# Kernel tuning notes

Measured on AMD Instinct MI355X. Metric: run time of the kernel, lower is better.

Reference implementation:

```python
import jax, jax.numpy as jnp
import numpy as np
import math

D_IN = 1024
D_OUT = 1024
NUM_HEADS = 16
HEAD_DIM = D_OUT // NUM_HEADS
B = 2
S = 4096


def setup_inputs() -> dict:
    key = jax.random.key(0)
    ks = jax.random.split(key, 6)
    x = jax.random.normal(ks[0], (B, S, D_IN), dtype=jnp.float32)
    # kaiming-uniform-ish scale for weights; exact init values don't matter for correctness
    bound = 1.0 / math.sqrt(D_IN)
    Wq = jax.random.uniform(ks[1], (D_OUT, D_IN), minval=-bound, maxval=bound, dtype=jnp.float32)
    Wk = jax.random.uniform(ks[2], (D_OUT, D_IN), minval=-bound, maxval=bound, dtype=jnp.float32)
    Wv = jax.random.uniform(ks[3], (D_OUT, D_IN), minval=-bound, maxval=bound, dtype=jnp.float32)
    Wo = jax.random.uniform(ks[4], (D_OUT, D_OUT), minval=-bound, maxval=bound, dtype=jnp.float32)
    bo = jax.random.uniform(ks[5], (D_OUT,), minval=-bound, maxval=bound, dtype=jnp.float32)
    return {"x": x, "Wq": Wq, "Wk": Wk, "Wv": Wv, "Wo": Wo, "bo": bo}


@jax.custom_vjp
def binarize(w):
    return jnp.sign(w)

def _bin_fwd(w):
    return jnp.sign(w), w

def _bin_bwd(w, g):
    # straight-through estimator: pass grad where |w| <= 1
    return (g * (jnp.abs(w) <= 1).astype(g.dtype),)

binarize.defvjp(_bin_fwd, _bin_bwd)


def reference(x, Wq, Wk, Wv, Wo, bo):
    b, n, _ = x.shape
    h, hd = NUM_HEADS, HEAD_DIM
    # binarized projections (torch F.linear: x @ W.T)
    q = (x @ binarize(Wq).T).reshape(b, n, h, hd).transpose(0, 2, 1, 3)  # [b,h,n,hd]
    k = (x @ binarize(Wk).T).reshape(b, n, h, hd).transpose(0, 2, 1, 3)
    v = (x @ binarize(Wv).T).reshape(b, n, h, hd).transpose(0, 2, 1, 3)
    scores = jnp.einsum('bhqd,bhkd->bhqk', q, k) / math.sqrt(hd)  # [b,h,n,n]
    causal = jnp.tril(jnp.ones((n, n), dtype=bool))
    scores = jnp.where(causal, scores, -jnp.inf)
    attn = jax.nn.softmax(scores, axis=-1)
    # dropout p=0.0 -> identity
    ctx = jnp.einsum('bhqk,bhkd->bqhd', attn, v).reshape(b, n, h * hd)
    return ctx @ binarize(Wo).T + bo
```

## Files before the change

kernel.cpp:

```cpp
#include <hip/hip_runtime.h>
#include <hip/hip_bf16.h>
#include <cstdint>
#include <cstddef>

#define S 4096
#define D 1024
#define H 16
#define HD 64
#define BATCH 2
#define M_TOK 8192
#define K2 2048

typedef short short8 __attribute__((ext_vector_type(8)));
typedef __bf16 bf16x8 __attribute__((ext_vector_type(8)));
typedef float f32x4 __attribute__((ext_vector_type(4)));
typedef unsigned int u32;

static __device__ __forceinline__ ushort f2bf(float f) {
  union { float f; uint32_t u; } v; v.f = f;
  uint32_t u = v.u + 0x7FFFu + ((v.u >> 16) & 1u);
  return (ushort)(u >> 16);
}
static __device__ __forceinline__ float bf2f(ushort h) {
  union { uint32_t u; float f; } v; v.u = ((uint32_t)h) << 16; return v.f;
}
static __device__ __forceinline__ uint32_t cvtpk(float lo, float hi) {
  uint32_t r;
  asm("v_cvt_pk_bf16_f32 %0, %1, %2" : "=v"(r) : "v"(lo), "v"(hi));
  return r;
}
static __device__ __forceinline__ float vexp2(float x) {
  float r;
  asm("v_exp_f32 %0, %1" : "=v"(r) : "v"(x));
  return r;
}
static __device__ __forceinline__ bf16x8 pack4(uint32_t a, uint32_t b, uint32_t c, uint32_t d) {
  union { uint32_t u[4]; bf16x8 v; } z;
  z.u[0] = a; z.u[1] = b; z.u[2] = c; z.u[3] = d;
  return z.v;
}
static __device__ __forceinline__ void gld16(const void* g, void* l) {
  __builtin_amdgcn_global_load_lds(
      (const __attribute__((address_space(1))) u32*)g,
      (__attribute__((address_space(3))) u32*)l, 16, 0, 0);
}
static __device__ __forceinline__ ushort sgn(float a) {
  return a > 0.f ? 0x3F80 : (a < 0.f ? 0xBF80 : 0);
}

__global__ void prep_x(const float* __restrict__ x, ushort* __restrict__ xcat) {
  int i = blockIdx.x * blockDim.x + threadIdx.x;
  const int total = M_TOK * 128;
  for (; i < total; i += gridDim.x * blockDim.x) {
    int row = i >> 7, c8 = (i & 127) * 8;
    const float* px = &x[(size_t)row * 1024 + c8];
    float4 a = *(const float4*)px;
    float4 b = *(const float4*)(px + 4);
    float va[8] = {a.x, a.y, a.z, a.w, b.x, b.y, b.z, b.w};
    union { ushort u[8]; short8 v; } Hh, Ll;
#pragma unroll
    for (int j = 0; j < 8; ++j) {
      ushort h = f2bf(va[j]);
      Hh.u[j] = h;
      Ll.u[j] = f2bf(va[j] - bf2f(h));
    }
    *(short8*)&xcat[(size_t)row * K2 + c8] = Hh.v;
    *(short8*)&xcat[(size_t)row * K2 + 1024 + c8] = Ll.v;
  }
}

__global__ void prep_w(const float* __restrict__ wq, const float* __restrict__ wk,
                       const float* __restrict__ wv, const float* __restrict__ wo,
                       ushort* __restrict__ wcat, ushort* __restrict__ wob) {
  int i = blockIdx.x * blockDim.x + threadIdx.x;
  const int total = (D * D) / 4;
  for (; i < total; i += gridDim.x * blockDim.x) {
    float4 a;
    union { ushort u[4]; uint2 v; } t;
    a = *(const float4*)&wq[i * 4];
    t.u[0] = sgn(a.x); t.u[1] = sgn(a.y); t.u[2] = sgn(a.z); t.u[3] = sgn(a.w);
    *(uint2*)&wcat[i * 4] = t.v;
    a = *(const float4*)&wk[i * 4];
    t.u[0] = sgn(a.x); t.u[1] = sgn(a.y); t.u[2] = sgn(a.z); t.u[3] = sgn(a.w);
    *(uint2*)&wcat[D * D + i * 4] = t.v;
    a = *(const float4*)&wv[i * 4];
    t.u[0] = sgn(a.x); t.u[1] = sgn(a.y); t.u[2] = sgn(a.z); t.u[3] = sgn(a.w);
    *(uint2*)&wcat[2 * D * D + i * 4] = t.v;
    a = *(const float4*)&wo[i * 4];
    t.u[0] = sgn(a.x); t.u[1] = sgn(a.y); t.u[2] = sgn(a.z); t.u[3] = sgn(a.w);
    *(uint2*)&wob[i * 4] = t.v;
  }
}

template<int EPI, int KK, int BROW>
__global__ __launch_bounds__(256) void gemm97(
    const ushort* __restrict__ A, const ushort* __restrict__ Bw,
    ushort* __restrict__ q_hi, ushort* __restrict__ q_lo,
    ushort* __restrict__ k_hi, ushort* __restrict__ k_lo,
    ushort* __restrict__ v_t,
    float* __restrict__ of, const float* __restrict__ bias)
{
  __shared__ ushort smA[128 * 32];
  __shared__ ushort smB[128 * 32];
  const int tid = threadIdx.x;
  const int l = tid & 63;
  const int w = tid >> 6;
  const int x = l & 15, g = l >> 4;
  const int wm = w >> 1, wn = w & 1;
  const int bm = blockIdx.x, bn = blockIdx.y;

  const ushort* gA[2]; const ushort* gB[2]; int ldso[2];
#pragma unroll
  for (int p = 0; p < 2; ++p) {
    int q = p * 256 + tid;
    gA[p] = &A[(size_t)(bm * 128 + (q >> 2)) * KK + (q & 3) * 8];
    gB[p] = &Bw[(size_t)(bn * 128 + (q >> 2)) * BROW + (q & 3) * 8];
    ldso[p] = (p * 256 + w * 64) * 8;
  }

  f32x4 acc[4][4] = {};

  for (int k0 = 0; k0 < KK; k0 += 32) {
    __syncthreads();
#pragma unroll
    for (int p = 0; p < 2; ++p) {
      gld16(gA[p] + k0, &smA[ldso[p]]);
      gld16(gB[p] + (k0 & (BROW - 1)), &smB[ldso[p]]);
    }
    __syncthreads();
    bf16x8 af[4], bf_[4];
#pragma unroll
    for (int m = 0; m < 4; ++m)
      af[m] = *(const bf16x8*)&smA[(wm * 64 + m * 16 + x) * 32 + g * 8];
#pragma unroll
    for (int n = 0; n < 4; ++n)
      bf_[n] = *(const bf16x8*)&smB[(wn * 64 + n * 16 + x) * 32 + g * 8];
#pragma unroll
    for (int m = 0; m < 4; ++m)
#pragma unroll
      for (int n = 0; n < 4; ++n)
        acc[m][n] = __builtin_amdgcn_mfma_f32_16x16x32_bf16(af[m], bf_[n], acc[m][n], 0, 0, 0);
  }

  if (EPI == 0) {
    const int proj = bn >> 3;
    ushort* oh = (proj == 0) ? q_hi : k_hi;
    ushort* ol = (proj == 0) ? q_lo : k_lo;
#pragma unroll
    for (int m = 0; m < 4; ++m)
#pragma unroll
      for (int n = 0; n < 4; ++n)
#pragma unroll
        for (int r = 0; r < 4; ++r) {
          int rowg = bm * 128 + wm * 64 + m * 16 + g * 4 + r;
          int colg = bn * 128 + wn * 64 + n * 16 + x;
          float v = acc[m][n][r];
          int bi = rowg >> 12, ntok = rowg & 4095;
          int cg = colg & 1023;
          int h = cg >> 6, hd = cg & 63;
          size_t bhb = (size_t)(bi * H + h) * (S * HD);
          if (proj < 2) {
            size_t off = bhb + (size_t)ntok * HD + hd;
            ushort hiv = f2bf(v);
            oh[off] = hiv;
            ol[off] = f2bf(v - bf2f(hiv));
          } else {
            int t5 = ntok & 31;
            int pos = ((t5 >> 2) & 3) * 8 + ((t5 >> 4) & 1) * 4 + (t5 & 3);
            v_t[bhb + (size_t)hd * S + (ntok & ~31) + pos] = f2bf(v);
          }
        }
  } else {
#pragma unroll
    for (int m = 0; m < 4; ++m)
#pragma unroll
      for (int n = 0; n < 4; ++n)
#pragma unroll
        for (int r = 0; r < 4; ++r) {
          int rowg = bm * 128 + wm * 64 + m * 16 + g * 4 + r;
          int colg = bn * 128 + wn * 64 + n * 16 + x;
          of[(size_t)rowg * D + colg] = acc[m][n][r] + bias[colg];
        }
  }
}

__global__ __launch_bounds__(256) void flash5(
    const ushort* __restrict__ qhi, const ushort* __restrict__ qlo,
    const ushort* __restrict__ khi, const ushort* __restrict__ klo,
    const ushort* __restrict__ vt, ushort* __restrict__ ctx)
{
  __shared__ ushort smKhi[2][64 * 64];
  __shared__ ushort smKlo[2][64 * 64];
  __shared__ ushort smVT[2][64 * 64];

  const int tid = threadIdx.x;
  const int l = tid & 63;
  const int w = tid >> 6;
  const int x = l & 15;
  const int g = l >> 4;
  const int bh = blockIdx.x;
  const int qt = (int)(gridDim.y - 1) - (int)blockIdx.y;
  const int qbase = qt * 128;
  const size_t qkbase = (size_t)bh * S * HD;

  int soff_k[2]; size_t soff_v[2]; int ldso[2];
#pragma unroll
  for (int p = 0; p < 2; ++p) {
    int q = p * 256 + tid;
    int rr = q >> 3;
    int sb = (q & 7) ^ (rr & 7);
    soff_k[p] = rr * HD + sb * 8;
    soff_v[p] = (size_t)rr * S + sb * 8;
    ldso[p] = (p * 256 + w * 64) * 8;
  }
  const ushort* khb = khi + qkbase;
  const ushort* klb = klo + qkbase;
  const ushort* vtb = vt + qkbase;

  bf16x8 bq[2][2][2];
#pragma unroll
  for (int qs = 0; qs < 2; ++qs) {
    int qrow = qbase + w * 32 + qs * 16 + x;
    size_t base = qkbase + (size_t)qrow * HD + g * 8;
    bq[qs][0][0] = *(const bf16x8*)&qhi[base];
    bq[qs][0][1] = *(const bf16x8*)&qhi[base + 32];
    bq[qs][1][0] = *(const bf16x8*)&qlo[base];
    bq[qs][1][1] = *(const bf16x8*)&qlo[base + 32];
  }

  float mrun[2] = {-1e30f, -1e30f};
  float lrun[2] = {0.f, 0.f};
  f32x4 oacc[2][4] = {};

  const int kvmax = (qbase + 127) >> 6;
  const int qmaxw = qbase + w * 32 + 31;
  const float C1 = 0.125f * 1.44269504f;
  const float TH = 8.0f / C1;

#pragma unroll
  for (int p = 0; p < 2; ++p) {
    gld16(khb + soff_k[p], &smKhi[0][ldso[p]]);
    gld16(klb + soff_k[p], &smKlo[0][ldso[p]]);
    gld16(vtb + soff_v[p], &smVT[0][ldso[p]]);
  }
  __syncthreads();

  int cur = 0;
  for (int kv = 0; kv <= kvmax; ++kv) {
    if (kv < kvmax) {
      const ushort* kh = khb + (size_t)(kv + 1) * (64 * HD);
      const ushort* kl = klb + (size_t)(kv + 1) * (64 * HD);
      const ushort* vp = vtb + (size_t)(kv + 1) * 64;
      int nb = cur ^ 1;
#pragma unroll
      for (int p = 0; p < 2; ++p) {
        gld16(kh + soff_k[p], &smKhi[nb][ldso[p]]);
        gld16(kl + soff_k[p], &smKlo[nb][ldso[p]]);
        gld16(vp + soff_v[p], &smVT[nb][ldso[p]]);
      }
    }

    if (kv * 64 <= qmaxw) {
      const ushort* bKhi = smKhi[cur];
      const ushort* bKlo = smKlo[cur];
      const ushort* bVT = smVT[cur];

      f32x4 scq[2][4];
      __builtin_amdgcn_s_setprio(1);
#pragma unroll
      for (int t = 0; t < 4; ++t) {
        f32x4 a0 = {}, a1 = {};
#pragma unroll
        for (int c = 0; c < 2; ++c) {
          int pb = (t * 16 + x) * 64 + ((4 * c + g) ^ (x & 7)) * 8;
          bf16x8 kH = *(const bf16x8*)&bKhi[pb];
          bf16x8 kL = *(const bf16x8*)&bKlo[pb];
          a0 = __builtin_amdgcn_mfma_f32_16x16x32_bf16(kH, bq[0][0][c], a0, 0, 0, 0);
          a0 = __builtin_amdgcn_mfma_f32_16x16x32_bf16(kL, bq[0][0][c], a0, 0, 0, 0);
          a0 = __builtin_amdgcn_mfma_f32_16x16x32_bf16(kH, bq[0][1][c], a0, 0, 0, 0);
          a1 = __builtin_amdgcn_mfma_f32_16x16x32_bf16(kH, bq[1][0][c], a1, 0, 0, 0);
          a1 = __builtin_amdgcn_mfma_f32_16x16x32_bf16(kL, bq[1][0][c], a1, 0, 0, 0);
          a1 = __builtin_amdgcn_mfma_f32_16x16x32_bf16(kH, bq[1][1][c], a1, 0, 0, 0);
        }
        scq[0][t] = a0; scq[1][t] = a1;
      }
      __builtin_amdgcn_s_setprio(0);

      const bool needmask = (kv * 64 + 63 > qbase + w * 32);
      uint32_t pbq[2][2][4];

#pragma unroll
      for (int qs = 0; qs < 2; ++qs) {
        if (needmask) {
          int qglob = qbase + w * 32 + qs * 16 + x;
          int kb = kv * 64 + 4 * g;
#pragma unroll
          for (int t = 0; t < 4; ++t)
#pragma unroll
            for (int r = 0; r < 4; ++r)
              if (kb + t * 16 + r > qglob) scq[qs][t][r] = -1e30f;
        }
        float mt[4];
#pragma unroll
        for (int t = 0; t < 4; ++t)
          mt[t] = fmaxf(fmaxf(scq[qs][t][0], scq[qs][t][1]),
                        fmaxf(scq[qs][t][2], scq[qs][t][3]));
        float mloc = fmaxf(fmaxf(mt[0], mt[1]), fmaxf(mt[2], mt[3]));
        if (__any(mloc > mrun[qs] + TH)) {
          mloc = fmaxf(mloc, __shfl_xor(mloc, 16));
          mloc = fmaxf(mloc, __shfl_xor(mloc, 32));
          float mnew = fmaxf(mrun[qs], mloc);
          float scal = vexp2((mrun[qs] - mnew) * C1);
          mrun[qs] = mnew;
          lrun[qs] *= scal;
#pragma unroll
          for (int dt = 0; dt < 4; ++dt) oacc[qs][dt] *= scal;
        }
        float mc = mrun[qs] * C1;
#pragma unroll
        for (int t = 0; t < 4; ++t)
#pragma unroll
          for (int r = 0; r < 4; ++r)
            scq[qs][t][r] = vexp2(scq[qs][t][r] * C1 - mc);
        float st[4];
#pragma unroll
        for (int t = 0; t < 4; ++t)
          st[t] = (scq[qs][t][0] + scq[qs][t][1]) + (scq[qs][t][2] + scq[qs][t][3]);
        lrun[qs] += (st[0] + st[1]) + (st[2] + st[3]);
#pragma unroll
        for (int c = 0; c < 2; ++c) {
          pbq[qs][c][0] = cvtpk(scq[qs][2 * c][0], scq[qs][2 * c][1]);
          pbq[qs][c][1] = cvtpk(scq[qs][2 * c][2], scq[qs][2 * c][3]);
          pbq[qs][c][2] = cvtpk(scq[qs][2 * c + 1][0], scq[qs][2 * c + 1][1]);
          pbq[qs][c][3] = cvtpk(scq[qs][2 * c + 1][2], scq[qs][2 * c + 1][3]);
        }
      }

      __builtin_amdgcn_s_setprio(1);
#pragma unroll
      for (int c = 0; c < 2; ++c)
#pragma unroll
        for (int dt = 0; dt < 4; ++dt) {
          bf16x8 vf = *(const bf16x8*)&bVT[(dt * 16 + x) * 64 + ((4 * c + g) ^ (x & 7)) * 8];
          oacc[0][dt] = __builtin_amdgcn_mfma_f32_16x16x32_bf16(
              vf, pack4(pbq[0][c][0], pbq[0][c][1], pbq[0][c][2], pbq[0][c][3]), oacc[0][dt], 0, 0, 0);
          oacc[1][dt] = __builtin_amdgcn_mfma_f32_16x16x32_bf16(
              vf, pack4(pbq[1][c][0], pbq[1][c][1], pbq[1][c][2], pbq[1][c][3]), oacc[1][dt], 0, 0, 0);
        }
      __builtin_amdgcn_s_setprio(0);
    }

    __syncthreads();
    cur ^= 1;
  }

  const int b = bh >> 4, h = bh & 15;
#pragma unroll
  for (int qs = 0; qs < 2; ++qs) {
    float ls = lrun[qs];
    ls += __shfl_xor(ls, 16);
    ls += __shfl_xor(ls, 32);
    float inv = 1.0f / ls;
    int tok = qbase + w * 32 + qs * 16 + x;
#pragma unroll
    for (int dt = 0; dt < 4; ++dt) {
      uint2 uu;
      uu.x = cvtpk(oacc[qs][dt][0] * inv, oacc[qs][dt][1] * inv);
      uu.y = cvtpk(oacc[qs][dt][2] * inv, oacc[qs][dt][3] * inv);
      *(uint2*)&ctx[(size_t)(b * S + tok) * D + h * 64 + dt * 16 + 4 * g] = uu;
    }
  }
}

extern "C" void kernel_launch(void* const* d_in, const int* in_sizes, int n_in,
                              void* d_out, int out_size, void* d_ws, size_t ws_size,
                              hipStream_t stream) {
  const float* x  = (const float*)d_in[0];
  const float* Wq = (const float*)d_in[1];
  const float* Wk = (const float*)d_in[2];
  const float* Wv = (const float*)d_in[3];
  const float* Wo = (const float*)d_in[4];
  const float* bo = (const float*)d_in[5];
  float* out = (float*)d_out;

  if (ws_size < (size_t)120 * 1024 * 1024) return;

  char* ws = (char*)d_ws;
  const size_t MB = 1024 * 1024;
  ushort* xcat = (ushort*)(ws);
  ushort* ctx  = (ushort*)(ws);
  ushort* wcat = (ushort*)(ws + 32 * MB);
  ushort* wob  = (ushort*)(ws + 38 * MB);
  ushort* qhi  = (ushort*)(ws + 40 * MB);
  ushort* qlo  = (ushort*)(ws + 56 * MB);
  ushort* khi  = (ushort*)(ws + 72 * MB);
  ushort* klo  = (ushort*)(ws + 88 * MB);
  ushort* vt   = (ushort*)(ws + 104 * MB);

  prep_x<<<2048, 256, 0, stream>>>(x, xcat);
  prep_w<<<1024, 256, 0, stream>>>(Wq, Wk, Wv, Wo, wcat, wob);

  gemm97<0, K2, 1024><<<dim3(64, 24), 256, 0, stream>>>(
      xcat, wcat, qhi, qlo, khi, klo, vt, nullptr, nullptr);

  flash5<<<dim3(BATCH * H, S / 128), 256, 0, stream>>>(qhi, qlo, khi, klo, vt, ctx);

  gemm97<2, 1024, 1024><<<dim3(64, 8), 256, 0, stream>>>(
      ctx, wob, nullptr, nullptr, nullptr, nullptr, nullptr, out, bo);
}
```

Before: 339.3 us.

## Pair complementary causal query tiles in one 512-thread flash block

Each flash-attention block now has 8 waves. Waves 0-3 handle query tile p and waves 4-7 handle tile 31-p, so every block does balanced causal work and the shared K/V tiles are loaded cooperatively across twice as many threads. This targets the load imbalance and tail effect of the triangular causal workload and halves the grid size. In exchange, waves on the short tile sit idle through the later KV iterations while still joining the barriers, and launch bounds now require 512 threads with 4 blocks per SM.

Measured after the change: 362.3 us. 1.07x slower.

```diff
diff --git a/kernel.cpp b/kernel.cpp
--- a/kernel.cpp
+++ b/kernel.cpp
@@ -184,7 +184,7 @@
   }
 }
 
-__global__ __launch_bounds__(256) void flash5(
+__global__ __launch_bounds__(512, 4) void flash6(
     const ushort* __restrict__ qhi, const ushort* __restrict__ qlo,
     const ushort* __restrict__ khi, const ushort* __restrict__ klo,
     const ushort* __restrict__ vt, ushort* __restrict__ ctx)
@@ -196,23 +196,21 @@
   const int tid = threadIdx.x;
   const int l = tid & 63;
   const int w = tid >> 6;
+  const int wl = w & 3;
   const int x = l & 15;
   const int g = l >> 4;
   const int bh = blockIdx.x;
-  const int qt = (int)(gridDim.y - 1) - (int)blockIdx.y;
-  const int qbase = qt * 128;
+  const int p = blockIdx.y;
+  const int qtw = (w < 4) ? p : (31 - p);
+  const int qbase = qtw * 128;
   const size_t qkbase = (size_t)bh * S * HD;
 
-  int soff_k[2]; size_t soff_v[2]; int ldso[2];
-#pragma unroll
-  for (int p = 0; p < 2; ++p) {
-    int q = p * 256 + tid;
-    int rr = q >> 3;
-    int sb = (q & 7) ^ (rr & 7);
-    soff_k[p] = rr * HD + sb * 8;
-    soff_v[p] = (size_t)rr * S + sb * 8;
-    ldso[p] = (p * 256 + w * 64) * 8;
-  }
+  const int rr = tid >> 3;
+  const int sb = (tid & 7) ^ (rr & 7);
+  const int soff_k = rr * HD + sb * 8;
+  const size_t soff_v = (size_t)rr * S + sb * 8;
+  const int ldso = w * 512;
+
   const ushort* khb = khi + qkbase;
   const ushort* klb = klo + qkbase;
   const ushort* vtb = vt + qkbase;
@@ -220,7 +218,7 @@
   bf16x8 bq[2][2][2];
 #pragma unroll
   for (int qs = 0; qs < 2; ++qs) {
-    int qrow = qbase + w * 32 + qs * 16 + x;
+    int qrow = qbase + wl * 32 + qs * 16 + x;
     size_t base = qkbase + (size_t)qrow * HD + g * 8;
     bq[qs][0][0] = *(const bf16x8*)&qhi[base];
     bq[qs][0][1] = *(const bf16x8*)&qhi[base + 32];
@@ -232,17 +230,14 @@
   float lrun[2] = {0.f, 0.f};
   f32x4 oacc[2][4] = {};
 
-  const int kvmax = (qbase + 127) >> 6;
-  const int qmaxw = qbase + w * 32 + 31;
+  const int kvmax = 2 * (31 - p) + 1;
+  const int qmaxw = qbase + wl * 32 + 31;
   const float C1 = 0.125f * 1.44269504f;
   const float TH = 8.0f / C1;
 
-#pragma unroll
-  for (int p = 0; p < 2; ++p) {
-    gld16(khb + soff_k[p], &smKhi[0][ldso[p]]);
-    gld16(klb + soff_k[p], &smKlo[0][ldso[p]]);
-    gld16(vtb + soff_v[p], &smVT[0][ldso[p]]);
-  }
+  gld16(khb + soff_k, &smKhi[0][ldso]);
+  gld16(klb + soff_k, &smKlo[0][ldso]);
+  gld16(vtb + soff_v, &smVT[0][ldso]);
   __syncthreads();
 
   int cur = 0;
@@ -252,12 +247,9 @@
       const ushort* kl = klb + (size_t)(kv + 1) * (64 * HD);
       const ushort* vp = vtb + (size_t)(kv + 1) * 64;
       int nb = cur ^ 1;
-#pragma unroll
-      for (int p = 0; p < 2; ++p) {
-        gld16(kh + soff_k[p], &smKhi[nb][ldso[p]]);
-        gld16(kl + soff_k[p], &smKlo[nb][ldso[p]]);
-        gld16(vp + soff_v[p], &smVT[nb][ldso[p]]);
-      }
+      gld16(kh + soff_k, &smKhi[nb][ldso]);
+      gld16(kl + soff_k, &smKlo[nb][ldso]);
+      gld16(vp + soff_v, &smVT[nb][ldso]);
     }
 
     if (kv * 64 <= qmaxw) {
@@ -286,13 +278,13 @@
       }
       __builtin_amdgcn_s_setprio(0);
 
-      const bool needmask = (kv * 64 + 63 > qbase + w * 32);
+      const bool needmask = (kv * 64 + 63 > qbase + wl * 32);
       uint32_t pbq[2][2][4];
 
 #pragma unroll
       for (int qs = 0; qs < 2; ++qs) {
         if (needmask) {
-          int qglob = qbase + w * 32 + qs * 16 + x;
+          int qglob = qbase + wl * 32 + qs * 16 + x;
           int kb = kv * 64 + 4 * g;
 #pragma unroll
           for (int t = 0; t < 4; ++t)
@@ -361,7 +353,7 @@
     ls += __shfl_xor(ls, 16);
     ls += __shfl_xor(ls, 32);
     float inv = 1.0f / ls;
-    int tok = qbase + w * 32 + qs * 16 + x;
+    int tok = qbase + wl * 32 + qs * 16 + x;
 #pragma unroll
     for (int dt = 0; dt < 4; ++dt) {
       uint2 uu;
@@ -403,7 +395,7 @@
   gemm97<0, K2, 1024><<<dim3(64, 24), 256, 0, stream>>>(
       xcat, wcat, qhi, qlo, khi, klo, vt, nullptr, nullptr);
 
-  flash5<<<dim3(BATCH * H, S / 128), 256, 0, stream>>>(qhi, qlo, khi, klo, vt, ctx);
+  flash6<<<dim3(BATCH * H, 16), 512, 0, stream>>>(qhi, qlo, khi, klo, vt, ctx);
 
   gemm97<2, 1024, 1024><<<dim3(64, 8), 256, 0, stream>>>(
       ctx, wob, nullptr, nullptr, nullptr, nullptr, nullptr, out, bo);
```

## Triple-buffer flash attention K/V tiles with one barrier per iteration

Applied to the files above, without the earlier changes.

The attention kernel goes from two to three LDS buffers for the K-hi, K-lo and V^T tiles. This lets each iteration use a single barrier, placed after an explicit vmcnt wait that leaves the next tile's loads in flight, instead of two __syncthreads. The goal is to cut barrier stalls and overlap global-to-LDS copies with MFMA work. LDS use per block rises by half, which may lower occupancy. The correctness of the partial vmcnt wait depends on the count of outstanding loads per thread.

Measured after the change: 341.8 us. Within noise of the previous version (+0.7%).

```diff
diff --git a/kernel.cpp b/kernel.cpp
--- a/kernel.cpp
+++ b/kernel.cpp
@@ -184,14 +184,14 @@
   }
 }
 
-__global__ __launch_bounds__(256) void flash5(
+__global__ __launch_bounds__(256) void flash9(
     const ushort* __restrict__ qhi, const ushort* __restrict__ qlo,
     const ushort* __restrict__ khi, const ushort* __restrict__ klo,
     const ushort* __restrict__ vt, ushort* __restrict__ ctx)
 {
-  __shared__ ushort smKhi[2][64 * 64];
-  __shared__ ushort smKlo[2][64 * 64];
-  __shared__ ushort smVT[2][64 * 64];
+  __shared__ ushort smKhi[3][64 * 64];
+  __shared__ ushort smKlo[3][64 * 64];
+  __shared__ ushort smVT[3][64 * 64];
 
   const int tid = threadIdx.x;
   const int l = tid & 63;
@@ -203,14 +203,15 @@
   const int qbase = qt * 128;
   const size_t qkbase = (size_t)bh * S * HD;
 
+  const int rr = tid >> 2;
   int soff_k[2]; size_t soff_v[2]; int ldso[2];
 #pragma unroll
   for (int p = 0; p < 2; ++p) {
     int q = p * 256 + tid;
-    int rr = q >> 3;
-    int sb = (q & 7) ^ (rr & 7);
-    soff_k[p] = rr * HD + sb * 8;
-    soff_v[p] = (size_t)rr * S + sb * 8;
+    int r2 = q >> 3;
+    int sb = (q & 7) ^ (r2 & 7);
+    soff_k[p] = r2 * HD + sb * 8;
+    soff_v[p] = (size_t)r2 * S + sb * 8;
     ldso[p] = (p * 256 + w * 64) * 8;
   }
   const ushort* khb = khi + qkbase;
@@ -243,27 +244,30 @@
     gld16(klb + soff_k[p], &smKlo[0][ldso[p]]);
     gld16(vtb + soff_v[p], &smVT[0][ldso[p]]);
   }
-  __syncthreads();
-
-  int cur = 0;
+
+  int cb = 0;
   for (int kv = 0; kv <= kvmax; ++kv) {
     if (kv < kvmax) {
       const ushort* kh = khb + (size_t)(kv + 1) * (64 * HD);
       const ushort* kl = klb + (size_t)(kv + 1) * (64 * HD);
       const ushort* vp = vtb + (size_t)(kv + 1) * 64;
-      int nb = cur ^ 1;
+      int nb = (cb == 2) ? 0 : cb + 1;
 #pragma unroll
       for (int p = 0; p < 2; ++p) {
         gld16(kh + soff_k[p], &smKhi[nb][ldso[p]]);
         gld16(kl + soff_k[p], &smKlo[nb][ldso[p]]);
         gld16(vp + soff_v[p], &smVT[nb][ldso[p]]);
       }
+      asm volatile("s_waitcnt vmcnt(6)" ::: "memory");
+    } else {
+      asm volatile("s_waitcnt vmcnt(0)" ::: "memory");
     }
+    __builtin_amdgcn_s_barrier();
 
     if (kv * 64 <= qmaxw) {
-      const ushort* bKhi = smKhi[cur];
-      const ushort* bKlo = smKlo[cur];
-      const ushort* bVT = smVT[cur];
+      const ushort* bKhi = smKhi[cb];
+      const ushort* bKlo = smKlo[cb];
+      const ushort* bVT = smVT[cb];
 
       f32x4 scq[2][4];
       __builtin_amdgcn_s_setprio(1);
@@ -350,8 +354,7 @@
       __builtin_amdgcn_s_setprio(0);
     }
 
-    __syncthreads();
-    cur ^= 1;
+    cb = (cb == 2) ? 0 : cb + 1;
   }
 
   const int b = bh >> 4, h = bh & 15;
@@ -403,7 +406,7 @@
   gemm97<0, K2, 1024><<<dim3(64, 24), 256, 0, stream>>>(
       xcat, wcat, qhi, qlo, khi, klo, vt, nullptr, nullptr);
 
-  flash5<<<dim3(BATCH * H, S / 128), 256, 0, stream>>>(qhi, qlo, khi, klo, vt, ctx);
+  flash9<<<dim3(BATCH * H, S / 128), 256, 0, stream>>>(qhi, qlo, khi, klo, vt, ctx);
 
   gemm97<2, 1024, 1024><<<dim3(64, 8), 256, 0, stream>>>(
       ctx, wob, nullptr, nullptr, nullptr, nullptr, nullptr, out, bo);
```

## Use persistent flash-attention blocks with an atomic work queue; split V projection GEMM

Applied to the files above, without the earlier changes.

The attention kernel becomes persistent: 768 blocks pull (head, query-tile) items from a global atomic counter, heaviest causal tiles first, to balance the triangular workload. The counter is zeroed with a memset before launch. The QKV projection is split into two GEMMs. The Q/K GEMM keeps the full 2048-wide K (hi/lo split input), while the V GEMM reads only the first 1024 columns, removing the redundant lo-part FLOPs for V. This adds an extra launch, a memset and atomic dispatch overhead.

New measurement: 339.8 us. No clear change (+0.1%).

```diff
diff --git a/kernel.cpp b/kernel.cpp
--- a/kernel.cpp
+++ b/kernel.cpp
@@ -92,7 +92,7 @@
   }
 }
 
-template<int EPI, int KK, int BROW>
+template<int EPI, int KK, int BROW, int AST>
 __global__ __launch_bounds__(256) void gemm97(
     const ushort* __restrict__ A, const ushort* __restrict__ Bw,
     ushort* __restrict__ q_hi, ushort* __restrict__ q_lo,
@@ -113,7 +113,7 @@
 #pragma unroll
   for (int p = 0; p < 2; ++p) {
     int q = p * 256 + tid;
-    gA[p] = &A[(size_t)(bm * 128 + (q >> 2)) * KK + (q & 3) * 8];
+    gA[p] = &A[(size_t)(bm * 128 + (q >> 2)) * AST + (q & 3) * 8];
     gB[p] = &Bw[(size_t)(bn * 128 + (q >> 2)) * BROW + (q & 3) * 8];
     ldso[p] = (p * 256 + w * 64) * 8;
   }
@@ -142,24 +142,26 @@
         acc[m][n] = __builtin_amdgcn_mfma_f32_16x16x32_bf16(af[m], bf_[n], acc[m][n], 0, 0, 0);
   }
 
-  if (EPI == 0) {
-    const int proj = bn >> 3;
-    ushort* oh = (proj == 0) ? q_hi : k_hi;
-    ushort* ol = (proj == 0) ? q_lo : k_lo;
-#pragma unroll
-    for (int m = 0; m < 4; ++m)
-#pragma unroll
-      for (int n = 0; n < 4; ++n)
-#pragma unroll
-        for (int r = 0; r < 4; ++r) {
-          int rowg = bm * 128 + wm * 64 + m * 16 + g * 4 + r;
-          int colg = bn * 128 + wn * 64 + n * 16 + x;
-          float v = acc[m][n][r];
+#pragma unroll
+  for (int m = 0; m < 4; ++m)
+#pragma unroll
+    for (int n = 0; n < 4; ++n)
+#pragma unroll
+      for (int r = 0; r < 4; ++r) {
+        int rowg = bm * 128 + wm * 64 + m * 16 + g * 4 + r;
+        int colg = bn * 128 + wn * 64 + n * 16 + x;
+        float v = acc[m][n][r];
+        if (EPI == 2) {
+          of[(size_t)rowg * D + colg] = v + bias[colg];
+        } else {
           int bi = rowg >> 12, ntok = rowg & 4095;
           int cg = colg & 1023;
           int h = cg >> 6, hd = cg & 63;
           size_t bhb = (size_t)(bi * H + h) * (S * HD);
-          if (proj < 2) {
+          if (EPI == 0) {
+            const int proj = bn >> 3;
+            ushort* oh = (proj == 0) ? q_hi : k_hi;
+            ushort* ol = (proj == 0) ? q_lo : k_lo;
             size_t off = bhb + (size_t)ntok * HD + hd;
             ushort hiv = f2bf(v);
             oh[off] = hiv;
@@ -170,204 +172,204 @@
             v_t[bhb + (size_t)hd * S + (ntok & ~31) + pos] = f2bf(v);
           }
         }
-  } else {
-#pragma unroll
-    for (int m = 0; m < 4; ++m)
-#pragma unroll
-      for (int n = 0; n < 4; ++n)
-#pragma unroll
-        for (int r = 0; r < 4; ++r) {
-          int rowg = bm * 128 + wm * 64 + m * 16 + g * 4 + r;
-          int colg = bn * 128 + wn * 64 + n * 16 + x;
-          of[(size_t)rowg * D + colg] = acc[m][n][r] + bias[colg];
-        }
-  }
-}
-
-__global__ __launch_bounds__(256) void flash5(
+      }
+}
+
+__global__ __launch_bounds__(256) void flash13(
     const ushort* __restrict__ qhi, const ushort* __restrict__ qlo,
     const ushort* __restrict__ khi, const ushort* __restrict__ klo,
-    const ushort* __restrict__ vt, ushort* __restrict__ ctx)
+    const ushort* __restrict__ vt, ushort* __restrict__ ctx,
+    u32* __restrict__ ctr)
 {
   __shared__ ushort smKhi[2][64 * 64];
   __shared__ ushort smKlo[2][64 * 64];
   __shared__ ushort smVT[2][64 * 64];
+  __shared__ int item_s;
 
   const int tid = threadIdx.x;
   const int l = tid & 63;
   const int w = tid >> 6;
   const int x = l & 15;
   const int g = l >> 4;
-  const int bh = blockIdx.x;
-  const int qt = (int)(gridDim.y - 1) - (int)blockIdx.y;
-  const int qbase = qt * 128;
-  const size_t qkbase = (size_t)bh * S * HD;
 
   int soff_k[2]; size_t soff_v[2]; int ldso[2];
 #pragma unroll
   for (int p = 0; p < 2; ++p) {
     int q = p * 256 + tid;
-    int rr = q >> 3;
-    int sb = (q & 7) ^ (rr & 7);
-    soff_k[p] = rr * HD + sb * 8;
-    soff_v[p] = (size_t)rr * S + sb * 8;
+    int r2 = q >> 3;
+    int sb = (q & 7) ^ (r2 & 7);
+    soff_k[p] = r2 * HD + sb * 8;
+    soff_v[p] = (size_t)r2 * S + sb * 8;
     ldso[p] = (p * 256 + w * 64) * 8;
   }
-  const ushort* khb = khi + qkbase;
-  const ushort* klb = klo + qkbase;
-  const ushort* vtb = vt + qkbase;
-
-  bf16x8 bq[2][2][2];
-#pragma unroll
-  for (int qs = 0; qs < 2; ++qs) {
-    int qrow = qbase + w * 32 + qs * 16 + x;
-    size_t base = qkbase + (size_t)qrow * HD + g * 8;
-    bq[qs][0][0] = *(const bf16x8*)&qhi[base];
-    bq[qs][0][1] = *(const bf16x8*)&qhi[base + 32];
-    bq[qs][1][0] = *(const bf16x8*)&qlo[base];
-    bq[qs][1][1] = *(const bf16x8*)&qlo[base + 32];
-  }
-
-  float mrun[2] = {-1e30f, -1e30f};
-  float lrun[2] = {0.f, 0.f};
-  f32x4 oacc[2][4] = {};
-
-  const int kvmax = (qbase + 127) >> 6;
-  const int qmaxw = qbase + w * 32 + 31;
   const float C1 = 0.125f * 1.44269504f;
   const float TH = 8.0f / C1;
 
-#pragma unroll
-  for (int p = 0; p < 2; ++p) {
-    gld16(khb + soff_k[p], &smKhi[0][ldso[p]]);
-    gld16(klb + soff_k[p], &smKlo[0][ldso[p]]);
-    gld16(vtb + soff_v[p], &smVT[0][ldso[p]]);
-  }
-  __syncthreads();
-
-  int cur = 0;
-  for (int kv = 0; kv <= kvmax; ++kv) {
-    if (kv < kvmax) {
-      const ushort* kh = khb + (size_t)(kv + 1) * (64 * HD);
-      const ushort* kl = klb + (size_t)(kv + 1) * (64 * HD);
-      const ushort* vp = vtb + (size_t)(kv + 1) * 64;
-      int nb = cur ^ 1;
-#pragma unroll
-      for (int p = 0; p < 2; ++p) {
-        gld16(kh + soff_k[p], &smKhi[nb][ldso[p]]);
-        gld16(kl + soff_k[p], &smKlo[nb][ldso[p]]);
-        gld16(vp + soff_v[p], &smVT[nb][ldso[p]]);
-      }
-    }
-
-    if (kv * 64 <= qmaxw) {
-      const ushort* bKhi = smKhi[cur];
-      const ushort* bKlo = smKlo[cur];
-      const ushort* bVT = smVT[cur];
-
-      f32x4 scq[2][4];
-      __builtin_amdgcn_s_setprio(1);
-#pragma unroll
-      for (int t = 0; t < 4; ++t) {
-        f32x4 a0 = {}, a1 = {};
-#pragma unroll
-        for (int c = 0; c < 2; ++c) {
-          int pb = (t * 16 + x) * 64 + ((4 * c + g) ^ (x & 7)) * 8;
-          bf16x8 kH = *(const bf16x8*)&bKhi[pb];
-          bf16x8 kL = *(const bf16x8*)&bKlo[pb];
-          a0 = __builtin_amdgcn_mfma_f32_16x16x32_bf16(kH, bq[0][0][c], a0, 0, 0, 0);
-          a0 = __builtin_amdgcn_mfma_f32_16x16x32_bf16(kL, bq[0][0][c], a0, 0, 0, 0);
-          a0 = __builtin_amdgcn_mfma_f32_16x16x32_bf16(kH, bq[0][1][c], a0, 0, 0, 0);
-          a1 = __builtin_amdgcn_mfma_f32_16x16x32_bf16(kH, bq[1][0][c], a1, 0, 0, 0);
-          a1 = __builtin_amdgcn_mfma_f32_16x16x32_bf16(kL, bq[1][0][c], a1, 0, 0, 0);
-          a1 = __builtin_amdgcn_mfma_f32_16x16x32_bf16(kH, bq[1][1][c], a1, 0, 0, 0);
-        }
-        scq[0][t] = a0; scq[1][t] = a1;
-      }
-      __builtin_amdgcn_s_setprio(0);
-
-      const bool needmask = (kv * 64 + 63 > qbase + w * 32);
-      uint32_t pbq[2][2][4];
-
-#pragma unroll
-      for (int qs = 0; qs < 2; ++qs) {
-        if (needmask) {
-          int qglob = qbase + w * 32 + qs * 16 + x;
-          int kb = kv * 64 + 4 * g;
-#pragma unroll
-          for (int t = 0; t < 4; ++t)
-#pragma unroll
-            for (int r = 0; r < 4; ++r)
-              if (kb + t * 16 + r > qglob) scq[qs][t][r] = -1e30f;
-        }
-        float mt[4];
-#pragma unroll
-        for (int t = 0; t < 4; ++t)
-          mt[t] = fmaxf(fmaxf(scq[qs][t][0], scq[qs][t][1]),
-                        fmaxf(scq[qs][t][2], scq[qs][t][3]));
-        float mloc = fmaxf(fmaxf(mt[0], mt[1]), fmaxf(mt[2], mt[3]));
-        if (__any(mloc > mrun[qs] + TH)) {
-          mloc = fmaxf(mloc, __shfl_xor(mloc, 16));
-          mloc = fmaxf(mloc, __shfl_xor(mloc, 32));
-          float mnew = fmaxf(mrun[qs], mloc);
-          float scal = vexp2((mrun[qs] - mnew) * C1);
-          mrun[qs] = mnew;
-          lrun[qs] *= scal;
-#pragma unroll
-          for (int dt = 0; dt < 4; ++dt) oacc[qs][dt] *= scal;
-        }
-        float mc = mrun[qs] * C1;
-#pragma unroll
-        for (int t = 0; t < 4; ++t)
-#pragma unroll
-          for (int r = 0; r < 4; ++r)
-            scq[qs][t][r] = vexp2(scq[qs][t][r] * C1 - mc);
-        float st[4];
-#pragma unroll
-        for (int t = 0; t < 4; ++t)
-          st[t] = (scq[qs][t][0] + scq[qs][t][1]) + (scq[qs][t][2] + scq[qs][t][3]);
-        lrun[qs] += (st[0] + st[1]) + (st[2] + st[3]);
-#pragma unroll
-        for (int c = 0; c < 2; ++c) {
-          pbq[qs][c][0] = cvtpk(scq[qs][2 * c][0], scq[qs][2 * c][1]);
-          pbq[qs][c][1] = cvtpk(scq[qs][2 * c][2], scq[qs][2 * c][3]);
-          pbq[qs][c][2] = cvtpk(scq[qs][2 * c + 1][0], scq[qs][2 * c + 1][1]);
-          pbq[qs][c][3] = cvtpk(scq[qs][2 * c + 1][2], scq[qs][2 * c + 1][3]);
+  for (;;) {
+    if (tid == 0) item_s = (int)atomicAdd(ctr, 1u);
+    __syncthreads();
+    const int item = item_s;
+    __syncthreads();
+    if (item >= 32 * 32) break;
+
+    const int bh = item & 31;
+    const int qt = 31 - (item >> 5);
+    const int qbase = qt * 128;
+    const size_t qkbase = (size_t)bh * S * HD;
+    const ushort* khb = khi + qkbase;
+    const ushort* klb = klo + qkbase;
+    const ushort* vtb = vt + qkbase;
+
+    bf16x8 bq[2][2][2];
+#pragma unroll
+    for (int qs = 0; qs < 2; ++qs) {
+      int qrow = qbase + w * 32 + qs * 16 + x;
+      size_t base = qkbase + (size_t)qrow * HD + g * 8;
+      bq[qs][0][0] = *(const bf16x8*)&qhi[base];
+      bq[qs][0][1] = *(const bf16x8*)&qhi[base + 32];
+      bq[qs][1][0] = *(const bf16x8*)&qlo[base];
+      bq[qs][1][1] = *(const bf16x8*)&qlo[base + 32];
+    }
+
+    float mrun[2] = {-1e30f, -1e30f};
+    float lrun[2] = {0.f, 0.f};
+    f32x4 oacc[2][4] = {};
+
+    const int kvmax = (qbase + 127) >> 6;
+    const int qmaxw = qbase + w * 32 + 31;
+
+#pragma unroll
+    for (int p = 0; p < 2; ++p) {
+      gld16(khb + soff_k[p], &smKhi[0][ldso[p]]);
+      gld16(klb + soff_k[p], &smKlo[0][ldso[p]]);
+      gld16(vtb + soff_v[p], &smVT[0][ldso[p]]);
+    }
+    __syncthreads();
+
+    int cur = 0;
+    for (int kv = 0; kv <= kvmax; ++kv) {
+      if (kv < kvmax) {
+        const ushort* kh = khb + (size_t)(kv + 1) * (64 * HD);
+        const ushort* kl = klb + (size_t)(kv + 1) * (64 * HD);
+        const ushort* vp = vtb + (size_t)(kv + 1) * 64;
+        int nb = cur ^ 1;
+#pragma unroll
+        for (int p = 0; p < 2; ++p) {
+          gld16(kh + soff_k[p], &smKhi[nb][ldso[p]]);
+          gld16(kl + soff_k[p], &smKlo[nb][ldso[p]]);
+          gld16(vp + soff_v[p], &smVT[nb][ldso[p]]);
         }
       }
 
-      __builtin_amdgcn_s_setprio(1);
-#pragma unroll
-      for (int c = 0; c < 2; ++c)
-#pragma unroll
-        for (int dt = 0; dt < 4; ++dt) {
-          bf16x8 vf = *(const bf16x8*)&bVT[(dt * 16 + x) * 64 + ((4 * c + g) ^ (x & 7)) * 8];
-          oacc[0][dt] = __builtin_amdgcn_mfma_f32_16x16x32_bf16(
-              vf, pack4(pbq[0][c][0], pbq[0][c][1], pbq[0][c][2], pbq[0][c][3]), oacc[0][dt], 0, 0, 0);
-          oacc[1][dt] = __builtin_amdgcn_mfma_f32_16x16x32_bf16(
-              vf, pack4(pbq[1][c][0], pbq[1][c][1], pbq[1][c][2], pbq[1][c][3]), oacc[1][dt], 0, 0, 0);
+      if (kv * 64 <= qmaxw) {
+        const ushort* bKhi = smKhi[cur];
+        const ushort* bKlo = smKlo[cur];
+        const ushort* bVT = smVT[cur];
+
+        f32x4 scq[2][4];
+        __builtin_amdgcn_s_setprio(1);
+#pragma unroll
+        for (int t = 0; t < 4; ++t) {
+          f32x4 a0 = {}, a1 = {};
+#pragma unroll
+          for (int c = 0; c < 2; ++c) {
+            int pb = (t * 16 + x) * 64 + ((4 * c + g) ^ (x & 7)) * 8;
+            bf16x8 kH = *(const bf16x8*)&bKhi[pb];
+            bf16x8 kL = *(const bf16x8*)&bKlo[pb];
+            a0 = __builtin_amdgcn_mfma_f32_16x16x32_bf16(kH, bq[0][0][c], a0, 0, 0, 0);
+            a0 = __builtin_amdgcn_mfma_f32_16x16x32_bf16(kL, bq[0][0][c], a0, 0, 0, 0);
+            a0 = __builtin_amdgcn_mfma_f32_16x16x32_bf16(kH, bq[0][1][c], a0, 0, 0, 0);
+            a1 = __builtin_amdgcn_mfma_f32_16x16x32_bf16(kH, bq[1][0][c], a1, 0, 0, 0);
+            a1 = __builtin_amdgcn_mfma_f32_16x16x32_bf16(kL, bq[1][0][c], a1, 0, 0, 0);
+            a1 = __builtin_amdgcn_mfma_f32_16x16x32_bf16(kH, bq[1][1][c], a1, 0, 0, 0);
+          }
+          scq[0][t] = a0; scq[1][t] = a1;
         }
-      __builtin_amdgcn_s_setprio(0);
-    }
-
-    __syncthreads();
-    cur ^= 1;
-  }
-
-  const int b = bh >> 4, h = bh & 15;
-#pragma unroll
-  for (int qs = 0; qs < 2; ++qs) {
-    float ls = lrun[qs];
-    ls += __shfl_xor(ls, 16);
-    ls += __shfl_xor(ls, 32);
-    float inv = 1.0f / ls;
-    int tok = qbase + w * 32 + qs * 16 + x;
-#pragma unroll
-    for (int dt = 0; dt < 4; ++dt) {
-      uint2 uu;
-      uu.x = cvtpk(oacc[qs][dt][0] * inv, oacc[qs][dt][1] * inv);
-      uu.y = cvtpk(oacc[qs][dt][2] * inv, oacc[qs][dt][3] * inv);
-      *(uint2*)&ctx[(size_t)(b * S + tok) * D + h * 64 + dt * 16 + 4 * g] = uu;
+        __builtin_amdgcn_s_setprio(0);
+
+        const bool needmask = (kv * 64 + 63 > qbase + w * 32);
+        uint32_t pbq[2][2][4];
+
+#pragma unroll
+        for (int qs = 0; qs < 2; ++qs) {
+          if (needmask) {
+            int qglob = qbase + w * 32 + qs * 16 + x;
+            int kb = kv * 64 + 4 * g;
+#pragma unroll
+            for (int t = 0; t < 4; ++t)
+#pragma unroll
+              for (int r = 0; r < 4; ++r)
+                if (kb + t * 16 + r > qglob) scq[qs][t][r] = -1e30f;
+          }
+          float mt[4];
+#pragma unroll
+          for (int t = 0; t < 4; ++t)
+            mt[t] = fmaxf(fmaxf(scq[qs][t][0], scq[qs][t][1]),
+                          fmaxf(scq[qs][t][2], scq[qs][t][3]));
+          float mloc = fmaxf(fmaxf(mt[0], mt[1]), fmaxf(mt[2], mt[3]));
+          if (__any(mloc > mrun[qs] + TH)) {
+            mloc = fmaxf(mloc, __shfl_xor(mloc, 16));
+            mloc = fmaxf(mloc, __shfl_xor(mloc, 32));
+            float mnew = fmaxf(mrun[qs], mloc);
+            float scal = vexp2((mrun[qs] - mnew) * C1);
+            mrun[qs] = mnew;
+            lrun[qs] *= scal;
+#pragma unroll
+            for (int dt = 0; dt < 4; ++dt) oacc[qs][dt] *= scal;
+          }
+          float mc = mrun[qs] * C1;
+#pragma unroll
+          for (int t = 0; t < 4; ++t)
+#pragma unroll
+            for (int r = 0; r < 4; ++r)
+              scq[qs][t][r] = vexp2(scq[qs][t][r] * C1 - mc);
+          float st[4];
+#pragma unroll
+          for (int t = 0; t < 4; ++t)
+            st[t] = (scq[qs][t][0] + scq[qs][t][1]) + (scq[qs][t][2] + scq[qs][t][3]);
+          lrun[qs] += (st[0] + st[1]) + (st[2] + st[3]);
+#pragma unroll
+          for (int c = 0; c < 2; ++c) {
+            pbq[qs][c][0] = cvtpk(scq[qs][2 * c][0], scq[qs][2 * c][1]);
+            pbq[qs][c][1] = cvtpk(scq[qs][2 * c][2], scq[qs][2 * c][3]);
+            pbq[qs][c][2] = cvtpk(scq[qs][2 * c + 1][0], scq[qs][2 * c + 1][1]);
+            pbq[qs][c][3] = cvtpk(scq[qs][2 * c + 1][2], scq[qs][2 * c + 1][3]);
+          }
+        }
+
+        __builtin_amdgcn_s_setprio(1);
+#pragma unroll
+        for (int c = 0; c < 2; ++c)
+#pragma unroll
+          for (int dt = 0; dt < 4; ++dt) {
+            bf16x8 vf = *(const bf16x8*)&bVT[(dt * 16 + x) * 64 + ((4 * c + g) ^ (x & 7)) * 8];
+            oacc[0][dt] = __builtin_amdgcn_mfma_f32_16x16x32_bf16(
+                vf, pack4(pbq[0][c][0], pbq[0][c][1], pbq[0][c][2], pbq[0][c][3]), oacc[0][dt], 0, 0, 0);
+            oacc[1][dt] = __builtin_amdgcn_mfma_f32_16x16x32_bf16(
+                vf, pack4(pbq[1][c][0], pbq[1][c][1], pbq[1][c][2], pbq[1][c][3]), oacc[1][dt], 0, 0, 0);
+          }
+        __builtin_amdgcn_s_setprio(0);
+      }
+
+      __syncthreads();
+      cur ^= 1;
+    }
+
+    const int b = bh >> 4, h = bh & 15;
+#pragma unroll
+    for (int qs = 0; qs < 2; ++qs) {
+      float ls = lrun[qs];
+      ls += __shfl_xor(ls, 16);
+      ls += __shfl_xor(ls, 32);
+      float inv = 1.0f / ls;
+      int tok = qbase + w * 32 + qs * 16 + x;
+#pragma unroll
+      for (int dt = 0; dt < 4; ++dt) {
+        uint2 uu;
+        uu.x = cvtpk(oacc[qs][dt][0] * inv, oacc[qs][dt][1] * inv);
+        uu.y = cvtpk(oacc[qs][dt][2] * inv, oacc[qs][dt][3] * inv);
+        *(uint2*)&ctx[(size_t)(b * S + tok) * D + h * 64 + dt * 16 + 4 * g] = uu;
+      }
     }
   }
 }
@@ -389,6 +391,7 @@
   const size_t MB = 1024 * 1024;
   ushort* xcat = (ushort*)(ws);
   ushort* ctx  = (ushort*)(ws);
+  u32*    ctr  = (u32*)(ws + 31 * MB);
   ushort* wcat = (ushort*)(ws + 32 * MB);
   ushort* wob  = (ushort*)(ws + 38 * MB);
   ushort* qhi  = (ushort*)(ws + 40 * MB);
@@ -400,11 +403,15 @@
   prep_x<<<2048, 256, 0, stream>>>(x, xcat);
   prep_w<<<1024, 256, 0, stream>>>(Wq, Wk, Wv, Wo, wcat, wob);
 
-  gemm97<0, K2, 1024><<<dim3(64, 24), 256, 0, stream>>>(
-      xcat, wcat, qhi, qlo, khi, klo, vt, nullptr, nullptr);
-
-  flash5<<<dim3(BATCH * H, S / 128), 256, 0, stream>>>(qhi, qlo, khi, klo, vt, ctx);
-
-  gemm97<2, 1024, 1024><<<dim3(64, 8), 256, 0, stream>>>(
+  gemm97<0, 2048, 1024, 2048><<<dim3(64, 16), 256, 0, stream>>>(
+      xcat, wcat, qhi, qlo, khi, klo, nullptr, nullptr, nullptr);
+  gemm97<1, 1024, 1024, 2048><<<dim3(64, 8), 256, 0, stream>>>(
+      xcat, wcat + 2 * D * D, nullptr, nullptr, nullptr, nullptr, vt, nullptr, nullptr);
+
+  hipMemsetAsync(ctr, 0, sizeof(u32), stream);
+
+  flash13<<<768, 256, 0, stream>>>(qhi, qlo, khi, klo, vt, ctx, ctr);
+
+  gemm97<2, 1024, 1024, 1024><<<dim3(64, 8), 256, 0, stream>>>(
       ctx, wob, nullptr, nullptr, nullptr, nullptr, nullptr, out, bo);
 }
```
